# Optimization experiments

Hardware: AMD Instinct MI355X
Metric: run time of the kernel (lower is better)

## Reference

```python
import jax, jax.numpy as jnp
import numpy as np

N_NODES = 100000


def _add_self_loops(edge_index, n):
    loop = jnp.arange(n, dtype=edge_index.dtype)
    src = jnp.concatenate([edge_index[0], loop])
    dst = jnp.concatenate([edge_index[1], loop])
    return src, dst


def _gcn_conv(x, src, dst, n, W, b):
    # PyG GCNConv: linear first, then sym-normalized aggregation, then bias.
    h = x @ W                                   # [N, out]
    deg = jnp.zeros((n,), h.dtype).at[dst].add(1.0)   # in-degree incl. self-loops
    dinv = jnp.where(deg > 0, jax.lax.rsqrt(deg), 0.0)
    norm = dinv[src] * dinv[dst]                # [E+N]
    msg = h[src] * norm[:, None]                # gather + scale
    out = jax.ops.segment_sum(msg, dst, num_segments=n)  # scatter-add
    return out + b


def setup_inputs() -> dict:
    key = jax.random.key(0)
    ks = jax.random.split(key, 9)
    n, d_in, d_h, d_out = N_NODES, 64, 64, 64
    x = jax.random.normal(ks[0], (n, d_in), jnp.float32)
    edge_index = jax.random.randint(ks[1], (2, 1200000), 0, n, jnp.int64)
    s = lambda k, sh: jax.random.normal(k, sh, jnp.float32) * (1.0 / np.sqrt(sh[0]))
    return {
        "x": x,
        "edge_index": edge_index,
        "W1": s(ks[2], (d_in, d_h)),
        "b1": jnp.zeros((d_h,), jnp.float32),
        "W2": s(ks[3], (d_h, d_out)),
        "b2": jnp.zeros((d_out,), jnp.float32),
        "Wl": s(ks[4], (d_out, d_out)),
        "bl": jnp.zeros((d_out,), jnp.float32),
    }


def reference(x, edge_index, W1, b1, W2, b2, Wl, bl):
    n = x.shape[0]
    src, dst = _add_self_loops(edge_index, n)
    h = _gcn_conv(x, src, dst, n, W1, b1)
    h = jax.nn.relu(h)
    h = _gcn_conv(h, src, dst, n, W2, b2)
    return h @ Wl + bl
```

## Files before the change

### kernel.cpp

```cpp
#include <hip/hip_runtime.h>
#include <hip/hip_bf16.h>


#define FEAT 64

typedef __attribute__((ext_vector_type(8))) short bf16x8;
typedef __attribute__((ext_vector_type(4))) float f32x4;
union BF8 { bf16x8 v; unsigned short u[8]; unsigned pk[4]; uint4 q; };

__device__ __forceinline__ unsigned short f2bf(float f) {
    unsigned u = __float_as_uint(f);
    return (unsigned short)((u + 0x7FFFu + ((u >> 16) & 1u)) >> 16);
}
__device__ __forceinline__ float bflo(unsigned u) { return __uint_as_float(u << 16); }
__device__ __forceinline__ float bfhi(unsigned u) { return __uint_as_float(u & 0xFFFF0000u); }
__device__ __forceinline__ unsigned pk2bf(float a, float b) {
    union { __hip_bfloat162 b; unsigned u; } cv;
    cv.b = __float22bfloat162_rn(make_float2(a, b));
    return cv.u;
}

__global__ void k_prepw(const float* __restrict__ W1, const float* __restrict__ W2,
                        const float* __restrict__ Wl, unsigned short* __restrict__ P,
                        int* __restrict__ bcnt) {
    if (blockIdx.x == 3) {
        if (threadIdx.x < 256) bcnt[threadIdx.x] = 0;
        return;
    }
    const float* W = (blockIdx.x == 0) ? W1 : (blockIdx.x == 1) ? W2 : Wl;
    unsigned short* p = P + blockIdx.x * 4096;
    for (int i = threadIdx.x; i < 4096; i += 256) {
        int c = i >> 10, s = (i >> 9) & 1, l = (i >> 3) & 63, j = i & 7;
        int k = s * 32 + ((l >> 4) << 3) + j;
        int col = ((l & 15) << 2) + c;
        p[i] = f2bf(W[k * 64 + col]);
    }
}

__global__ void __launch_bounds__(256)
k_bhist(const int* __restrict__ dst, int* __restrict__ bcnt, int E) {
    __shared__ int h[256];
    int tid = threadIdx.x;
    h[tid] = 0;
    __syncthreads();
    int stride = gridDim.x * 256;
    for (int e = blockIdx.x * 256 + tid; e < E; e += stride)
        atomicAdd(&h[dst[e] >> 9], 1);
    __syncthreads();
    if (h[tid]) atomicAdd(&bcnt[tid], h[tid]);
}

__global__ void k_bscan(const int* __restrict__ bcnt, int* __restrict__ bbase,
                        int* __restrict__ bcur) {
    __shared__ int s[256];
    int t = threadIdx.x;
    int v = bcnt[t];
    s[t] = v;
    __syncthreads();
    for (int off = 1; off < 256; off <<= 1) {
        int x = (t >= off) ? s[t - off] : 0;
        __syncthreads();
        s[t] += x;
        __syncthreads();
    }
    int ex = s[t] - v;
    bbase[t] = ex;
    bcur[t] = ex;
    if (t == 255) bbase[256] = s[255];
}

__global__ void __launch_bounds__(256)
k_part(const int* __restrict__ src, const int* __restrict__ dst,
       int* __restrict__ bcur, unsigned* __restrict__ pass1, int E) {
    __shared__ unsigned pk[4096];
    __shared__ unsigned char bk[4096];
    __shared__ int h[256];
    __shared__ int cur[256];
    int tid = threadIdx.x;
    h[tid] = 0;
    __syncthreads();
    int base = blockIdx.x * 4096;
#pragma unroll
    for (int i = 0; i < 16; ++i) {
        int li = i * 256 + tid;
        int e = base + li;
        if (e < E) {
            int s = src[e], d = dst[e];
            int b = d >> 9;
            pk[li] = ((unsigned)s << 9) | ((unsigned)d & 511u);
            bk[li] = (unsigned char)b;
            atomicAdd(&h[b], 1);
        } else {
            bk[li] = 255;
            pk[li] = 0xFFFFFFFFu;
        }
    }
    __syncthreads();
    {
        int c = h[tid];
        int run = c ? atomicAdd(&bcur[tid], c) : 0;
        cur[tid] = run;
    }
    __syncthreads();
#pragma unroll
    for (int i = 0; i < 16; ++i) {
        int li = i * 256 + tid;
        int e = base + li;
        if (e < E) {
            int b = bk[li];
            int pos = atomicAdd(&cur[b], 1);
            pass1[pos] = pk[li];
        }
    }
}

__global__ void __launch_bounds__(512)
k_csr(const unsigned* __restrict__ pass1, const int* __restrict__ bbase,
      int* __restrict__ offs, float* __restrict__ dinv, int* __restrict__ esrc,
      int n, int E) {
    __shared__ int hist[512];
    __shared__ int cur[512];
    int tid = threadIdx.x;
    int b = blockIdx.x;
    hist[tid] = 0;
    __syncthreads();
    int beg = bbase[b], end = bbase[b + 1];
    for (int j = beg + tid; j < end; j += 512)
        atomicAdd(&hist[pass1[j] & 511u], 1);
    __syncthreads();
    int v = hist[tid];
    for (int off = 1; off < 512; off <<= 1) {
        int x = (tid >= off) ? hist[tid - off] : 0;
        __syncthreads();
        hist[tid] += x;
        __syncthreads();
    }
    int excl = hist[tid] - v;
    int node = (b << 9) + tid;
    if (node < n) {
        offs[node] = beg + excl;
        dinv[node] = rsqrtf((float)v + 1.0f);
    }
    cur[tid] = excl;
    if (b == 0 && tid == 0) offs[n] = E;
    __syncthreads();
    for (int j = beg + tid; j < end; j += 512) {
        unsigned u = pass1[j];
        int loc = (int)(u & 511u);
        int r = atomicAdd(&cur[loc], 1);
        esrc[beg + r] = (int)(u >> 9);
    }
}

template <bool IN_BF16, bool OUT_F32, bool SCALE>
__global__ void __launch_bounds__(256)
k_gemm_mfma(const void* __restrict__ Xv, const unsigned short* __restrict__ Wpk,
            const float* __restrict__ bias, const float* __restrict__ rowscale,
            void* __restrict__ Hv, int n) {
    int lane = threadIdx.x & 63;
    int wid = (blockIdx.x << 2) + (threadIdx.x >> 6);
    int nw = gridDim.x << 2;
    int T = (n + 15) >> 4;
    BF8 bfr[8];
    const uint4* wp = (const uint4*)Wpk;
#pragma unroll
    for (int f = 0; f < 8; ++f) bfr[f].q = wp[f * 64 + lane];
    int mrow = lane & 15, kq = lane >> 4, colb = lane & 15;
    float4 bv4 = make_float4(0.f, 0.f, 0.f, 0.f);
    if (OUT_F32) bv4 = ((const float4*)bias)[colb];
    for (int t = wid; t < T; t += nw) {
        int rb = t << 4;
        int row = rb + mrow;
        bool ok = row < n;
        BF8 a0, a1;
        if (IN_BF16) {
            const uint4* xr = (const uint4*)((const unsigned short*)Xv + ((unsigned)row << 6));
            a0.q = ok ? xr[kq]     : make_uint4(0, 0, 0, 0);
            a1.q = ok ? xr[kq + 4] : make_uint4(0, 0, 0, 0);
        } else {
            const float4* xr = (const float4*)((const float*)Xv + ((unsigned)row << 6));
            float4 z = make_float4(0.f, 0.f, 0.f, 0.f);
            float4 p0 = ok ? xr[kq * 2]     : z;
            float4 p1 = ok ? xr[kq * 2 + 1] : z;
            float4 p2 = ok ? xr[8 + kq * 2] : z;
            float4 p3 = ok ? xr[8 + kq * 2 + 1] : z;
            a0.pk[0] = pk2bf(p0.x, p0.y); a0.pk[1] = pk2bf(p0.z, p0.w);
            a0.pk[2] = pk2bf(p1.x, p1.y); a0.pk[3] = pk2bf(p1.z, p1.w);
            a1.pk[0] = pk2bf(p2.x, p2.y); a1.pk[1] = pk2bf(p2.z, p2.w);
            a1.pk[2] = pk2bf(p3.x, p3.y); a1.pk[3] = pk2bf(p3.z, p3.w);
        }
        f32x4 acc0 = {0.f, 0.f, 0.f, 0.f}, acc1 = acc0, acc2 = acc0, acc3 = acc0;
        acc0 = __builtin_amdgcn_mfma_f32_16x16x32_bf16(a0.v, bfr[0].v, acc0, 0, 0, 0);
        acc0 = __builtin_amdgcn_mfma_f32_16x16x32_bf16(a1.v, bfr[1].v, acc0, 0, 0, 0);
        acc1 = __builtin_amdgcn_mfma_f32_16x16x32_bf16(a0.v, bfr[2].v, acc1, 0, 0, 0);
        acc1 = __builtin_amdgcn_mfma_f32_16x16x32_bf16(a1.v, bfr[3].v, acc1, 0, 0, 0);
        acc2 = __builtin_amdgcn_mfma_f32_16x16x32_bf16(a0.v, bfr[4].v, acc2, 0, 0, 0);
        acc2 = __builtin_amdgcn_mfma_f32_16x16x32_bf16(a1.v, bfr[5].v, acc2, 0, 0, 0);
        acc3 = __builtin_amdgcn_mfma_f32_16x16x32_bf16(a0.v, bfr[6].v, acc3, 0, 0, 0);
        acc3 = __builtin_amdgcn_mfma_f32_16x16x32_bf16(a1.v, bfr[7].v, acc3, 0, 0, 0);
        int rowb = rb + (kq << 2);
        if (OUT_F32) {
            float* O = (float*)Hv;
#pragma unroll
            for (int i = 0; i < 4; ++i) {
                if (rowb + i >= n) break;
                unsigned ro = (unsigned)(rowb + i) << 6;
                float4 o = make_float4(acc0[i] + bv4.x, acc1[i] + bv4.y,
                                       acc2[i] + bv4.z, acc3[i] + bv4.w);
                *(float4*)(O + ro + (colb << 2)) = o;
            }
        } else {
            unsigned short* O = (unsigned short*)Hv;
#pragma unroll
            for (int i = 0; i < 4; ++i) {
                if (rowb + i >= n) break;
                float sc = SCALE ? rowscale[rowb + i] : 1.0f;
                unsigned ro = (unsigned)(rowb + i) << 6;
                uint2 o = make_uint2(pk2bf(acc0[i] * sc, acc1[i] * sc),
                                     pk2bf(acc2[i] * sc, acc3[i] * sc));
                *(uint2*)(O + ro + (colb << 2)) = o;
            }
        }
    }
}

template <bool RELU>
__global__ void __launch_bounds__(256)
k_agg(const int* __restrict__ offs, const int* __restrict__ esrc,
      const float* __restrict__ dinv, const unsigned short* __restrict__ Hs,
      const float* __restrict__ bias, unsigned short* __restrict__ out, int n) {
    int lane = threadIdx.x & 63;
    int h8 = lane & 7;
    int node = blockIdx.x * 32 + ((threadIdx.x >> 6) << 3) + (lane >> 3);
    bool nok = node < n;
    int beg = 0, end = 0;
    if (nok) { beg = offs[node]; end = offs[node + 1]; }
    float a0 = 0.f, a1 = 0.f, a2 = 0.f, a3 = 0.f, a4 = 0.f, a5 = 0.f, a6 = 0.f, a7 = 0.f;
    int j = beg;
    int s0 = 0, s1 = 0;
    float w0 = 0.f, w1 = 0.f;
    if (j < end)     { s0 = esrc[j];     w0 = 1.f; }
    if (j + 1 < end) { s1 = esrc[j + 1]; w1 = 1.f; }
    while (__ballot(j < end)) {
        uint4 h0 = *(const uint4*)(Hs + ((unsigned)s0 << 6) + (h8 << 3));
        uint4 h1 = *(const uint4*)(Hs + ((unsigned)s1 << 6) + (h8 << 3));
        int jn = j + 2;
        int t0 = s0, t1 = s1;
        float v0 = 0.f, v1 = 0.f;
        if (jn < end)     { t0 = esrc[jn];     v0 = 1.f; }
        if (jn + 1 < end) { t1 = esrc[jn + 1]; v1 = 1.f; }
        a0 = fmaf(bflo(h0.x), w0, a0); a1 = fmaf(bfhi(h0.x), w0, a1);
        a2 = fmaf(bflo(h0.y), w0, a2); a3 = fmaf(bfhi(h0.y), w0, a3);
        a4 = fmaf(bflo(h0.z), w0, a4); a5 = fmaf(bfhi(h0.z), w0, a5);
        a6 = fmaf(bflo(h0.w), w0, a6); a7 = fmaf(bfhi(h0.w), w0, a7);
        a0 = fmaf(bflo(h1.x), w1, a0); a1 = fmaf(bfhi(h1.x), w1, a1);
        a2 = fmaf(bflo(h1.y), w1, a2); a3 = fmaf(bfhi(h1.y), w1, a3);
        a4 = fmaf(bflo(h1.z), w1, a4); a5 = fmaf(bfhi(h1.z), w1, a5);
        a6 = fmaf(bflo(h1.w), w1, a6); a7 = fmaf(bfhi(h1.w), w1, a7);
        j = jn; s0 = t0; s1 = t1; w0 = v0; w1 = v1;
    }
    if (nok) {
        float dd = dinv[node];
        uint4 sv = *(const uint4*)(Hs + ((unsigned)node << 6) + (h8 << 3));
        const float4* b4 = (const float4*)bias;
        float4 bA = b4[h8 * 2], bB = b4[h8 * 2 + 1];
        float r0 = (a0 + bflo(sv.x)) * dd + bA.x;
        float r1 = (a1 + bfhi(sv.x)) * dd + bA.y;
        float r2 = (a2 + bflo(sv.y)) * dd + bA.z;
        float r3 = (a3 + bfhi(sv.y)) * dd + bA.w;
        float r4 = (a4 + bflo(sv.z)) * dd + bB.x;
        float r5 = (a5 + bfhi(sv.z)) * dd + bB.y;
        float r6 = (a6 + bflo(sv.w)) * dd + bB.z;
        float r7 = (a7 + bfhi(sv.w)) * dd + bB.w;
        if (RELU) {
            r0 = fmaxf(r0, 0.f); r1 = fmaxf(r1, 0.f); r2 = fmaxf(r2, 0.f); r3 = fmaxf(r3, 0.f);
            r4 = fmaxf(r4, 0.f); r5 = fmaxf(r5, 0.f); r6 = fmaxf(r6, 0.f); r7 = fmaxf(r7, 0.f);
        }
        uint4 o = make_uint4(pk2bf(r0, r1), pk2bf(r2, r3), pk2bf(r4, r5), pk2bf(r6, r7));
        *(uint4*)(out + ((unsigned)node << 6) + (h8 << 3)) = o;
    }
}

extern "C" void kernel_launch(void* const* d_in, const int* in_sizes, int n_in,
                              void* d_out, int out_size, void* d_ws, size_t ws_size,
                              hipStream_t stream) {
    const float* x  = (const float*)d_in[0];
    const int*   ei = (const int*)d_in[1];
    const float* W1 = (const float*)d_in[2];
    const float* b1 = (const float*)d_in[3];
    const float* W2 = (const float*)d_in[4];
    const float* b2 = (const float*)d_in[5];
    const float* Wl = (const float*)d_in[6];
    const float* bl = (const float*)d_in[7];
    float* out = (float*)d_out;

    const int n = in_sizes[0] / FEAT;
    const int E = in_sizes[1] / 2;
    const int* src = ei;
    const int* dst = ei + E;

    const int B = 256;
    const int NB = (n + 511) >> 9;
    const int pblocks = (E + 4095) / 4096;
    const int agg_blocks  = (n + 31) / 32;
    const int T = (n + 15) / 16;
    const int gemm_blocks = (T + 7) / 8;

    char* w = (char*)d_ws;
    int*   bcnt     = (int*)w;              w += 256 * 4;
    int*   bbase    = (int*)w;              w += 260 * 4;
    int*   bcur     = (int*)w;              w += 256 * 4;
    int*   offs     = (int*)w;              w += ((size_t)n + 4) * 4;
    float* dinv     = (float*)w;            w += (size_t)n * 4;
    w = (char*)(((uintptr_t)w + 15) & ~(uintptr_t)15);
    unsigned short* Wpk = (unsigned short*)w;  w += 3 * 4096 * 2;
    unsigned* pass1 = (unsigned*)w;         w += (size_t)E * 4;
    int*   esrc     = (int*)w;              w += (size_t)E * 4;
    unsigned short* bufA = (unsigned short*)w;  w += (size_t)n * FEAT * 2;
    unsigned short* bufB = (unsigned short*)w;

    k_prepw<<<dim3(4), dim3(B), 0, stream>>>(W1, W2, Wl, Wpk, bcnt);

    k_bhist<<<dim3(256), dim3(B), 0, stream>>>(dst, bcnt, E);
    k_bscan<<<dim3(1), dim3(B), 0, stream>>>(bcnt, bbase, bcur);
    k_part<<<dim3(pblocks), dim3(B), 0, stream>>>(src, dst, bcur, pass1, E);
    k_csr<<<dim3(NB), dim3(512), 0, stream>>>(pass1, bbase, offs, dinv, esrc, n, E);

    k_gemm_mfma<false, false, true><<<dim3(gemm_blocks), dim3(B), 0, stream>>>(x, Wpk, nullptr, dinv, bufA, n);
    k_agg<true><<<dim3(agg_blocks), dim3(B), 0, stream>>>(offs, esrc, dinv, bufA, b1, bufB, n);

    k_gemm_mfma<true, false, true><<<dim3(gemm_blocks), dim3(B), 0, stream>>>(bufB, Wpk + 4096, nullptr, dinv, bufA, n);
    k_agg<false><<<dim3(agg_blocks), dim3(B), 0, stream>>>(offs, esrc, dinv, bufA, b2, bufB, n);

    k_gemm_mfma<true, true, false><<<dim3(gemm_blocks), dim3(B), 0, stream>>>(bufB, Wpk + 8192, bl, nullptr, out, n);
}
```

Baseline: 248.5 us.

## Store bf16 features in four 16-column planes and aggregate one plane per block

The intermediate bf16 feature buffers now use a planar layout: four contiguous planes of 16 features, 32 bytes per node per plane. GEMM reads and writes are remapped to this layout. The aggregation kernel now launches four times as many blocks, each handling one plane for 64 nodes, with 4 lanes per node and 4 edges unrolled per iteration. The aim is to shrink each plane's gather working set so it fits better in L2/MALL cache during the random neighbour gathers. The cost is that each edge index list is read four times and each gather is a smaller 8-byte load.

```diff
diff --git a/kernel.cpp b/kernel.cpp
--- a/kernel.cpp
+++ b/kernel.cpp
@@ -161,6 +161,7 @@
     int wid = (blockIdx.x << 2) + (threadIdx.x >> 6);
     int nw = gridDim.x << 2;
     int T = (n + 15) >> 4;
+    size_t ps = (size_t)n * 16;
     BF8 bfr[8];
     const uint4* wp = (const uint4*)Wpk;
 #pragma unroll
@@ -174,9 +175,12 @@
         bool ok = row < n;
         BF8 a0, a1;
         if (IN_BF16) {
-            const uint4* xr = (const uint4*)((const unsigned short*)Xv + ((unsigned)row << 6));
-            a0.q = ok ? xr[kq]     : make_uint4(0, 0, 0, 0);
-            a1.q = ok ? xr[kq + 4] : make_uint4(0, 0, 0, 0);
+            const unsigned short* X = (const unsigned short*)Xv;
+            const unsigned short* r0p =
+                X + (size_t)(kq >> 1) * ps + ((unsigned)row << 4) + ((kq & 1) << 3);
+            uint4 z4 = make_uint4(0, 0, 0, 0);
+            a0.q = ok ? *(const uint4*)r0p            : z4;
+            a1.q = ok ? *(const uint4*)(r0p + 2 * ps) : z4;
         } else {
             const float4* xr = (const float4*)((const float*)Xv + ((unsigned)row << 6));
             float4 z = make_float4(0.f, 0.f, 0.f, 0.f);
@@ -211,14 +215,14 @@
             }
         } else {
             unsigned short* O = (unsigned short*)Hv;
+            unsigned short* ob = O + (size_t)(colb >> 2) * ps + ((colb & 3) << 2);
 #pragma unroll
             for (int i = 0; i < 4; ++i) {
                 if (rowb + i >= n) break;
                 float sc = SCALE ? rowscale[rowb + i] : 1.0f;
-                unsigned ro = (unsigned)(rowb + i) << 6;
                 uint2 o = make_uint2(pk2bf(acc0[i] * sc, acc1[i] * sc),
                                      pk2bf(acc2[i] * sc, acc3[i] * sc));
-                *(uint2*)(O + ro + (colb << 2)) = o;
+                *(uint2*)(ob + ((unsigned)(rowb + i) << 4)) = o;
             }
         }
     }
@@ -228,56 +232,64 @@
 __global__ void __launch_bounds__(256)
 k_agg(const int* __restrict__ offs, const int* __restrict__ esrc,
       const float* __restrict__ dinv, const unsigned short* __restrict__ Hs,
-      const float* __restrict__ bias, unsigned short* __restrict__ out, int n) {
+      const float* __restrict__ bias, unsigned short* __restrict__ out,
+      int n, int nb1) {
     int lane = threadIdx.x & 63;
-    int h8 = lane & 7;
-    int node = blockIdx.x * 32 + ((threadIdx.x >> 6) << 3) + (lane >> 3);
+    int l4 = lane & 3;
+    int p = blockIdx.x / nb1;
+    int nb = blockIdx.x - p * nb1;
+    int node = nb * 64 + ((threadIdx.x >> 6) << 4) + (lane >> 2);
     bool nok = node < n;
     int beg = 0, end = 0;
     if (nok) { beg = offs[node]; end = offs[node + 1]; }
-    float a0 = 0.f, a1 = 0.f, a2 = 0.f, a3 = 0.f, a4 = 0.f, a5 = 0.f, a6 = 0.f, a7 = 0.f;
+    size_t ps = (size_t)n * 16;
+    const unsigned short* HP = Hs + (size_t)p * ps;
+    float a0 = 0.f, a1 = 0.f, a2 = 0.f, a3 = 0.f;
     int j = beg;
-    int s0 = 0, s1 = 0;
-    float w0 = 0.f, w1 = 0.f;
-    if (j < end)     { s0 = esrc[j];     w0 = 1.f; }
+    int s0 = 0, s1 = 0, s2 = 0, s3 = 0;
+    float w0 = 0.f, w1 = 0.f, w2 = 0.f, w3 = 0.f;
+    if (j     < end) { s0 = esrc[j];     w0 = 1.f; }
     if (j + 1 < end) { s1 = esrc[j + 1]; w1 = 1.f; }
+    if (j + 2 < end) { s2 = esrc[j + 2]; w2 = 1.f; }
+    if (j + 3 < end) { s3 = esrc[j + 3]; w3 = 1.f; }
     while (__ballot(j < end)) {
-        uint4 h0 = *(const uint4*)(Hs + ((unsigned)s0 << 6) + (h8 << 3));
-        uint4 h1 = *(const uint4*)(Hs + ((unsigned)s1 << 6) + (h8 << 3));
-        int jn = j + 2;
-        int t0 = s0, t1 = s1;
-        float v0 = 0.f, v1 = 0.f;
-        if (jn < end)     { t0 = esrc[jn];     v0 = 1.f; }
+        uint2 h0 = *(const uint2*)(HP + ((unsigned)s0 << 4) + (l4 << 2));
+        uint2 h1 = *(const uint2*)(HP + ((unsigned)s1 << 4) + (l4 << 2));
+        uint2 h2 = *(const uint2*)(HP + ((unsigned)s2 << 4) + (l4 << 2));
+        uint2 h3 = *(const uint2*)(HP + ((unsigned)s3 << 4) + (l4 << 2));
+        int jn = j + 4;
+        int t0 = s0, t1 = s1, t2 = s2, t3 = s3;
+        float v0 = 0.f, v1 = 0.f, v2 = 0.f, v3 = 0.f;
+        if (jn     < end) { t0 = esrc[jn];     v0 = 1.f; }
         if (jn + 1 < end) { t1 = esrc[jn + 1]; v1 = 1.f; }
+        if (jn + 2 < end) { t2 = esrc[jn + 2]; v2 = 1.f; }
+        if (jn + 3 < end) { t3 = esrc[jn + 3]; v3 = 1.f; }
         a0 = fmaf(bflo(h0.x), w0, a0); a1 = fmaf(bfhi(h0.x), w0, a1);
         a2 = fmaf(bflo(h0.y), w0, a2); a3 = fmaf(bfhi(h0.y), w0, a3);
-        a4 = fmaf(bflo(h0.z), w0, a4); a5 = fmaf(bfhi(h0.z), w0, a5);
-        a6 = fmaf(bflo(h0.w), w0, a6); a7 = fmaf(bfhi(h0.w), w0, a7);
         a0 = fmaf(bflo(h1.x), w1, a0); a1 = fmaf(bfhi(h1.x), w1, a1);
         a2 = fmaf(bflo(h1.y), w1, a2); a3 = fmaf(bfhi(h1.y), w1, a3);
-        a4 = fmaf(bflo(h1.z), w1, a4); a5 = fmaf(bfhi(h1.z), w1, a5);
-        a6 = fmaf(bflo(h1.w), w1, a6); a7 = fmaf(bfhi(h1.w), w1, a7);
-        j = jn; s0 = t0; s1 = t1; w0 = v0; w1 = v1;
+        a0 = fmaf(bflo(h2.x), w2, a0); a1 = fmaf(bfhi(h2.x), w2, a1);
+        a2 = fmaf(bflo(h2.y), w2, a2); a3 = fmaf(bfhi(h2.y), w2, a3);
+        a0 = fmaf(bflo(h3.x), w3, a0); a1 = fmaf(bfhi(h3.x), w3, a1);
+        a2 = fmaf(bflo(h3.y), w3, a2); a3 = fmaf(bfhi(h3.y), w3, a3);
+        j = jn;
+        s0 = t0; s1 = t1; s2 = t2; s3 = t3;
+        w0 = v0; w1 = v1; w2 = v2; w3 = v3;
     }
     if (nok) {
         float dd = dinv[node];
-        uint4 sv = *(const uint4*)(Hs + ((unsigned)node << 6) + (h8 << 3));
-        const float4* b4 = (const float4*)bias;
-        float4 bA = b4[h8 * 2], bB = b4[h8 * 2 + 1];
-        float r0 = (a0 + bflo(sv.x)) * dd + bA.x;
-        float r1 = (a1 + bfhi(sv.x)) * dd + bA.y;
-        float r2 = (a2 + bflo(sv.y)) * dd + bA.z;
-        float r3 = (a3 + bfhi(sv.y)) * dd + bA.w;
-        float r4 = (a4 + bflo(sv.z)) * dd + bB.x;
-        float r5 = (a5 + bfhi(sv.z)) * dd + bB.y;
-        float r6 = (a6 + bflo(sv.w)) * dd + bB.z;
-        float r7 = (a7 + bfhi(sv.w)) * dd + bB.w;
+        uint2 sv = *(const uint2*)(HP + ((unsigned)node << 4) + (l4 << 2));
+        float4 b4 = ((const float4*)bias)[(p << 2) + l4];
+        float r0 = (a0 + bflo(sv.x)) * dd + b4.x;
+        float r1 = (a1 + bfhi(sv.x)) * dd + b4.y;
+        float r2 = (a2 + bflo(sv.y)) * dd + b4.z;
+        float r3 = (a3 + bfhi(sv.y)) * dd + b4.w;
         if (RELU) {
-            r0 = fmaxf(r0, 0.f); r1 = fmaxf(r1, 0.f); r2 = fmaxf(r2, 0.f); r3 = fmaxf(r3, 0.f);
-            r4 = fmaxf(r4, 0.f); r5 = fmaxf(r5, 0.f); r6 = fmaxf(r6, 0.f); r7 = fmaxf(r7, 0.f);
-        }
-        uint4 o = make_uint4(pk2bf(r0, r1), pk2bf(r2, r3), pk2bf(r4, r5), pk2bf(r6, r7));
-        *(uint4*)(out + ((unsigned)node << 6) + (h8 << 3)) = o;
+            r0 = fmaxf(r0, 0.f); r1 = fmaxf(r1, 0.f);
+            r2 = fmaxf(r2, 0.f); r3 = fmaxf(r3, 0.f);
+        }
+        uint2 o = make_uint2(pk2bf(r0, r1), pk2bf(r2, r3));
+        *(uint2*)(out + (size_t)p * ps + ((unsigned)node << 4) + (l4 << 2)) = o;
     }
 }
 
@@ -302,7 +314,8 @@
     const int B = 256;
     const int NB = (n + 511) >> 9;
     const int pblocks = (E + 4095) / 4096;
-    const int agg_blocks  = (n + 31) / 32;
+    const int nb1 = (n + 63) / 64;
+    const int agg_blocks = 4 * nb1;
     const int T = (n + 15) / 16;
     const int gemm_blocks = (T + 7) / 8;
 
@@ -327,10 +340,10 @@
     k_csr<<<dim3(NB), dim3(512), 0, stream>>>(pass1, bbase, offs, dinv, esrc, n, E);
 
     k_gemm_mfma<false, false, true><<<dim3(gemm_blocks), dim3(B), 0, stream>>>(x, Wpk, nullptr, dinv, bufA, n);
-    k_agg<true><<<dim3(agg_blocks), dim3(B), 0, stream>>>(offs, esrc, dinv, bufA, b1, bufB, n);
+    k_agg<true><<<dim3(agg_blocks), dim3(B), 0, stream>>>(offs, esrc, dinv, bufA, b1, bufB, n, nb1);
 
     k_gemm_mfma<true, false, true><<<dim3(gemm_blocks), dim3(B), 0, stream>>>(bufB, Wpk + 4096, nullptr, dinv, bufA, n);
-    k_agg<false><<<dim3(agg_blocks), dim3(B), 0, stream>>>(offs, esrc, dinv, bufA, b2, bufB, n);
+    k_agg<false><<<dim3(agg_blocks), dim3(B), 0, stream>>>(offs, esrc, dinv, bufA, b2, bufB, n, nb1);
 
     k_gemm_mfma<true, true, false><<<dim3(gemm_blocks), dim3(B), 0, stream>>>(bufB, Wpk + 8192, bl, nullptr, out, n);
 }
```

Measured after the change: 271.7 us. 1.09x slower.
